# Performance work log

Hardware: AMD Instinct MI355X
Metric: run time of the kernel (lower is better)

Reference implementation:

```python
import jax, jax.numpy as jnp
import numpy as np

NUM_HEADS = 12


def _rel_lookup(rel_pos, size):
    # q_size == k_size == size, table length == 2*size-1: pure gather, no interp
    idx = jnp.arange(size)[:, None] - jnp.arange(size)[None, :] + (size - 1)
    return rel_pos[idx]  # (size, size, head_dim)


def setup_inputs() -> dict:
    key = jax.random.key(0)
    ks = jax.random.split(key, 7)
    B, H, W, C = 8, 32, 32, 768
    return {
        "x": jax.random.normal(ks[0], (B, H, W, C), dtype=jnp.float32),
        "w_qkv": jax.random.normal(ks[1], (C, 3 * C), dtype=jnp.float32) * 0.02,
        "b_qkv": jax.random.normal(ks[2], (3 * C,), dtype=jnp.float32) * 0.02,
        "w_proj": jax.random.normal(ks[3], (C, C), dtype=jnp.float32) * 0.02,
        "b_proj": jax.random.normal(ks[4], (C,), dtype=jnp.float32) * 0.02,
        "rel_pos_h": jax.random.normal(ks[5], (2 * H - 1, C // NUM_HEADS), dtype=jnp.float32) * 0.02,
        "rel_pos_w": jax.random.normal(ks[6], (2 * W - 1, C // NUM_HEADS), dtype=jnp.float32) * 0.02,
    }


def reference(x, w_qkv, b_qkv, w_proj, b_proj, rel_pos_h, rel_pos_w):
    B, H, W, C = x.shape
    nh = NUM_HEADS
    hd = C // nh
    scale = hd ** -0.5

    qkv = x @ w_qkv + b_qkv  # (B,H,W,3C)
    qkv = qkv.reshape(B, H * W, 3, nh, hd).transpose(2, 0, 3, 1, 4)
    qkv = qkv.reshape(3, B * nh, H * W, hd)
    q, k, v = qkv[0], qkv[1], qkv[2]  # each (B*nh, HW, hd)

    attn = jnp.einsum('bqd,bkd->bqk', q * scale, k)  # (B*nh, HW, HW)

    Rh = _rel_lookup(rel_pos_h, H)  # (H,H,hd)
    Rw = _rel_lookup(rel_pos_w, W)  # (W,W,hd)
    r_q = q.reshape(B * nh, H, W, hd)
    rel_h = jnp.einsum('bhwc,hkc->bhwk', r_q, Rh)  # (B*nh,H,W,H)
    rel_w = jnp.einsum('bhwc,wkc->bhwk', r_q, Rw)  # (B*nh,H,W,W)
    attn = (attn.reshape(B * nh, H, W, H, W)
            + rel_h[:, :, :, :, None]
            + rel_w[:, :, :, None, :]).reshape(B * nh, H * W, H * W)

    attn = jax.nn.softmax(attn, axis=-1)
    out = jnp.einsum('bqk,bkd->bqd', attn, v)  # (B*nh, HW, hd)
    out = out.reshape(B, nh, H, W, hd).transpose(0, 2, 3, 1, 4).reshape(B, H, W, C)
    return out @ w_proj + b_proj
```

## Files before the change

kernel.cpp:

```cpp
#include <hip/hip_runtime.h>

typedef unsigned short u16;
typedef unsigned int u32;
typedef __attribute__((ext_vector_type(8))) short short8;
typedef __attribute__((ext_vector_type(4))) float f32x4;
typedef __attribute__((ext_vector_type(4))) u32 u32x4;

__device__ __forceinline__ u16 f2bf(float f) {
  u32 u = __float_as_uint(f);
  return (u16)((u + 0x7FFFu + ((u >> 16) & 1u)) >> 16);
}
__device__ __forceinline__ float bf2f(u16 u) { return __uint_as_float(((u32)u) << 16); }
__device__ __forceinline__ f32x4 zero4() { f32x4 z = {0.f, 0.f, 0.f, 0.f}; return z; }

__device__ __forceinline__ u32 cvt_pk_bf16(float lo, float hi) {
  u32 r;
  asm("v_cvt_pk_bf16_f32 %0, %1, %2" : "=v"(r) : "v"(lo), "v"(hi));
  return r;
}

__device__ __forceinline__ void g2lds16(const void* g, void* l) {
  __builtin_amdgcn_global_load_lds((const __attribute__((address_space(1))) void*)g,
                                   (__attribute__((address_space(3))) void*)l, 16, 0, 0);
}

#define LOG2E 1.44269504088896340736f

__global__ __launch_bounds__(256) void cvt_x_kernel(const float* __restrict__ in,
                                                    u16* __restrict__ out, int n4) {
  int i = blockIdx.x * 256 + threadIdx.x;
  if (i >= n4) return;
  float4 v = ((const float4*)in)[i];
  ushort4 o;
  o.x = f2bf(v.x); o.y = f2bf(v.y); o.z = f2bf(v.z); o.w = f2bf(v.w);
  ((ushort4*)out)[i] = o;
}

__global__ __launch_bounds__(256) void transp_cvt_kernel(const float* __restrict__ in,
                                                         u16* __restrict__ out, int K, int N) {
  __shared__ float t[32][33];
  int n0 = blockIdx.x * 32, k0 = blockIdx.y * 32;
  int tx = threadIdx.x & 31, ty = threadIdx.x >> 5;
#pragma unroll
  for (int r = 0; r < 4; ++r)
    t[ty + r * 8][tx] = in[(size_t)(k0 + ty + r * 8) * N + n0 + tx];
  __syncthreads();
#pragma unroll
  for (int r = 0; r < 4; ++r)
    out[(size_t)(n0 + ty + r * 8) * K + k0 + tx] = f2bf(t[tx][ty + r * 8]);
}

template <int EPI>
__global__ __launch_bounds__(256, 3) void gemm_bt_kernel(
    const u16* __restrict__ A, const u16* __restrict__ Bt, const float* __restrict__ bias,
    int M, int N, int K,
    u16* __restrict__ q_out, u16* __restrict__ k_out, u16* __restrict__ vT_out,
    float* __restrict__ f_out) {
  __shared__ __align__(16) u16 As[2 * 128 * 32];
  __shared__ __align__(16) u16 Bs[2 * 128 * 32];
  const int tid = threadIdx.x;
  const int w = tid >> 6, lane = tid & 63;

  const int nwg = gridDim.x * gridDim.y;
  const int flat = blockIdx.y * gridDim.x + blockIdx.x;
  const int wg = (flat & 7) * (nwg >> 3) + (flat >> 3);
  const int bx = wg % gridDim.x, by = wg / gridDim.x;
  const int m0 = by * 128, n0 = bx * 128;
  const int wm0 = (w >> 1) * 64, wn0 = (w & 1) * 64;

  f32x4 acc[4][4];
#pragma unroll
  for (int i = 0; i < 4; ++i)
#pragma unroll
    for (int j = 0; j < 4; ++j) acc[i][j] = zero4();

  const int sRow = lane >> 2;
  const int sChunk = ((lane & 3) ^ ((lane >> 3) & 3)) * 8;
  const int cw = ((lane >> 4) << 4) ^ (((lane >> 1) & 3) << 4);
  const int g = lane >> 4, lc = lane & 15;
  const int lr = g << 2;

#define GSTAGE(buf, ktS)                                                                   \
  do {                                                                                     \
    _Pragma("unroll") for (int jj = 0; jj < 4; ++jj) {                                     \
      int i = w + jj * 4;                                                                  \
      if (i < 8)                                                                           \
        g2lds16(A + (size_t)(m0 + i * 16 + sRow) * K + (ktS) + sChunk,                     \
                (char*)As + (buf) * 8192 + i * 1024);                                      \
      else                                                                                 \
        g2lds16(Bt + (size_t)(n0 + (i - 8) * 16 + sRow) * K + (ktS) + sChunk,              \
                (char*)Bs + (buf) * 8192 + (i - 8) * 1024);                                \
    }                                                                                      \
  } while (0)

  const int nk = K >> 5;
  GSTAGE(0, 0);
  GSTAGE(1, 32);
  asm volatile("s_waitcnt vmcnt(4)" ::: "memory");
  __builtin_amdgcn_sched_barrier(0);
  __builtin_amdgcn_s_barrier();

  for (int kti = 0; kti < nk; ++kti) {
    const int cur = kti & 1;
    short8 af[4], bfr[4];
#pragma unroll
    for (int r = 0; r < 4; ++r) {
      af[r] = *(const short8*)((const char*)As + cur * 8192 + (wm0 + r * 16 + lc) * 64 + cw);
      bfr[r] = *(const short8*)((const char*)Bs + cur * 8192 + (wn0 + r * 16 + lc) * 64 + cw);
    }
    __builtin_amdgcn_s_setprio(1);
#pragma unroll
    for (int i = 0; i < 4; ++i)
#pragma unroll
      for (int j = 0; j < 4; ++j)
        acc[i][j] = __builtin_amdgcn_mfma_f32_16x16x32_bf16(af[i], bfr[j], acc[i][j], 0, 0, 0);
    __builtin_amdgcn_s_setprio(0);

    asm volatile("s_waitcnt lgkmcnt(0)" ::: "memory");
    __builtin_amdgcn_sched_barrier(0);
    __builtin_amdgcn_s_barrier();

    if (kti + 2 < nk) {
      GSTAGE(cur, (kti + 2) << 5);
      asm volatile("s_waitcnt vmcnt(4)" ::: "memory");
    } else {
      asm volatile("s_waitcnt vmcnt(0)" ::: "memory");
    }
    __builtin_amdgcn_sched_barrier(0);
    __builtin_amdgcn_s_barrier();
  }
#undef GSTAGE

#pragma unroll
  for (int j = 0; j < 4; ++j) {
    int n = n0 + wn0 + j * 16 + lc;
    float bv = bias[n];
    if (EPI == 0) {
      int three = n / 768;
      int rem = n - three * 768;
      int head = rem >> 6, d = rem & 63;
#pragma unroll
      for (int i = 0; i < 4; ++i) {
        if (three == 2) {
          int t0 = ((m0 + wm0 + i * 16 + lr) & 1023);
          int bb = (m0 + wm0 + i * 16 + lr) >> 10;
          size_t bh = (size_t)bb * 12 + head;
          ushort4 ov;
          ov.x = f2bf(acc[i][j][0] + bv);
          ov.y = f2bf(acc[i][j][1] + bv);
          ov.z = f2bf(acc[i][j][2] + bv);
          ov.w = f2bf(acc[i][j][3] + bv);
          *(ushort4*)(vT_out + (bh * 64 + d) * 1024 + t0) = ov;
        } else {
#pragma unroll
          for (int r = 0; r < 4; ++r) {
            int m = m0 + wm0 + i * 16 + lr + r;
            int bb = m >> 10, t = m & 1023;
            size_t bh = (size_t)bb * 12 + head;
            float val = acc[i][j][r] + bv;
            if (three == 0)
              q_out[(bh * 1024 + t) * 64 + d] = f2bf(val * (0.125f * LOG2E));
            else
              k_out[(bh * 1024 + t) * 64 + d] = f2bf(val);
          }
        }
      }
    } else {
#pragma unroll
      for (int i = 0; i < 4; ++i)
#pragma unroll
        for (int r = 0; r < 4; ++r) {
          int m = m0 + wm0 + i * 16 + lr + r;
          f_out[(size_t)m * N + n] = acc[i][j][r] + bv;
        }
    }
  }
}

__global__ __launch_bounds__(256) void rel_kernel(const u16* __restrict__ qs,
                                                  const float* __restrict__ rph,
                                                  const float* __restrict__ rpw,
                                                  float* __restrict__ relh,
                                                  float* __restrict__ relw) {
  __shared__ __align__(16) float Ts[63 * 68];
  __shared__ __align__(16) u16 Qs[32 * 72];
  const int tid = threadIdx.x;
  const int h = blockIdx.x, bh = blockIdx.y;
  const int mode = blockIdx.z;
  const float* table = mode ? rpw : rph;
  float* out = mode ? relw : relh;
  for (int i = tid; i < (63 * 64) / 4; i += 256) {
    float4 v = ((const float4*)table)[i];
    int row = i >> 4, col = (i & 15) * 4;
    *(float4*)(Ts + row * 68 + col) = v;
  }
  const u16* qrow = qs + ((size_t)bh * 1024 + h * 32) * 64;
  for (int i = tid; i < (32 * 64) / 8; i += 256) {
    uint4 v = ((const uint4*)qrow)[i];
    int row = i >> 3, col = (i & 7) * 8;
    *(uint4*)(Qs + row * 72 + col) = v;
  }
  __syncthreads();
  const int w = tid >> 3;
  const int kx = tid & 7;
  const int base = mode ? w : h;
  float acc0 = 0.f, acc1 = 0.f, acc2 = 0.f, acc3 = 0.f;
  const u16* qp = Qs + w * 72;
#pragma unroll
  for (int dc = 0; dc < 8; ++dc) {
    uint4 qv = *(const uint4*)(qp + dc * 8);
    float qf[8];
    qf[0] = bf2f((u16)(qv.x & 0xffff)); qf[1] = bf2f((u16)(qv.x >> 16));
    qf[2] = bf2f((u16)(qv.y & 0xffff)); qf[3] = bf2f((u16)(qv.y >> 16));
    qf[4] = bf2f((u16)(qv.z & 0xffff)); qf[5] = bf2f((u16)(qv.z >> 16));
    qf[6] = bf2f((u16)(qv.w & 0xffff)); qf[7] = bf2f((u16)(qv.w >> 16));
#pragma unroll
    for (int jj = 0; jj < 4; ++jj) {
      int row = base - (kx + 8 * jj) + 31;
      const float* tp = Ts + row * 68 + dc * 8;
      float4 p0 = ((const float4*)tp)[0];
      float4 p1 = ((const float4*)tp)[1];
      float s = qf[0] * p0.x + qf[1] * p0.y + qf[2] * p0.z + qf[3] * p0.w +
                qf[4] * p1.x + qf[5] * p1.y + qf[6] * p1.z + qf[7] * p1.w;
      if (jj == 0) acc0 += s;
      else if (jj == 1) acc1 += s;
      else if (jj == 2) acc2 += s;
      else acc3 += s;
    }
  }
  float* op = out + ((size_t)bh * 1024 + h * 32 + w) * 32 + kx;
  op[0] = acc0 * 8.f;
  op[8] = acc1 * 8.f;
  op[16] = acc2 * 8.f;
  op[24] = acc3 * 8.f;
}

__global__ __launch_bounds__(256) void flash_kernel(
    const u16* __restrict__ qs, const u16* __restrict__ kb, const u16* __restrict__ vT,
    const float* __restrict__ relh, const float* __restrict__ relw, u16* __restrict__ ao) {
  __shared__ __align__(16) u16 Ks[2 * 64 * 64];
  __shared__ __align__(16) u16 Vs[2 * 64 * 64];
  __shared__ __align__(16) float RhS[64 * 33];
  __shared__ __align__(16) u32 PpT[4][32 * 20];
  const int tid = threadIdx.x, wv = tid >> 6, lane = tid & 63;
  const int nwg = gridDim.x * gridDim.y;
  const int flat = blockIdx.y * gridDim.x + blockIdx.x;
  const int wg = (flat & 7) * (nwg >> 3) + (flat >> 3);
  const int qt = wg & 15, bh = wg >> 4;
  const int q0 = qt * 64;
  const int g = lane >> 4, lc = lane & 15;

  const float* rh_g = relh + ((size_t)bh * 1024 + q0) * 32;
  for (int i = tid; i < 64 * 32; i += 256) RhS[(i >> 5) * 33 + (i & 31)] = rh_g[i];

  const size_t qbase = ((size_t)bh * 1024 + q0 + wv * 16 + lc) * 64;
  short8 aq0 = *(const short8*)(qs + qbase + g * 8);
  short8 aq1 = *(const short8*)(qs + qbase + 32 + g * 8);

  const float* rwp = relw + ((size_t)bh * 1024 + q0 + wv * 16 + lc) * 32 + 4 * g;
  float4 rw0 = *(const float4*)(rwp);
  float4 rw1 = *(const float4*)(rwp + 16);
  float rwr[8] = {rw0.x, rw0.y, rw0.z, rw0.w, rw1.x, rw1.y, rw1.z, rw1.w};

  f32x4 o[4];
#pragma unroll
  for (int ct = 0; ct < 4; ++ct) o[ct] = zero4();
  float lsum = 0.f;
  const int rhbase = (wv * 16 + lc) * 33;

  const int stgRow = lane >> 3;
  const int stgChunk = ((lane & 7) ^ (lane >> 3)) * 8;
  u32* pt = &PpT[wv][0];

#define STAGE(buf, ktS)                                                                   \
  do {                                                                                    \
    const int k0s = (ktS) * 64;                                                           \
    _Pragma("unroll") for (int jj = 0; jj < 4; ++jj) {                                    \
      int i = wv + jj * 4;                                                                \
      if (i < 8)                                                                          \
        g2lds16(kb + ((size_t)bh * 1024 + k0s + i * 8 + stgRow) * 64 + stgChunk,          \
                (char*)Ks + (buf) * 8192 + i * 1024);                                     \
      else                                                                                \
        g2lds16(vT + ((size_t)bh * 64 + (i - 8) * 8 + stgRow) * 1024 + k0s + stgChunk,    \
                (char*)Vs + (buf) * 8192 + (i - 8) * 1024);                               \
    }                                                                                     \
  } while (0)

  STAGE(0, 0);
  __syncthreads();

  for (int kt = 0; kt < 16; ++kt) {
    const int cur = kt & 1;
    if (kt < 15) STAGE(cur ^ 1, kt + 1);

    f32x4 s[4];
    __builtin_amdgcn_s_setprio(1);
#pragma unroll
    for (int ct = 0; ct < 4; ++ct) {
      int key = ct * 16 + lc;
      int sw = (key & 7) << 4;
      const char* kp = (const char*)Ks + cur * 8192 + key * 128;
      short8 kf0 = *(const short8*)(kp + ((g * 16) ^ sw));
      short8 kf1 = *(const short8*)(kp + ((64 + g * 16) ^ sw));
      f32x4 z = zero4();
      z = __builtin_amdgcn_mfma_f32_16x16x32_bf16(kf0, aq0, z, 0, 0, 0);
      z = __builtin_amdgcn_mfma_f32_16x16x32_bf16(kf1, aq1, z, 0, 0, 0);
      s[ct] = z;
    }
    __builtin_amdgcn_s_setprio(0);

    float rh0 = RhS[rhbase + kt * 2 + 0];
    float rh1 = RhS[rhbase + kt * 2 + 1];
    float pr[4][4];
#pragma unroll
    for (int ct = 0; ct < 4; ++ct)
#pragma unroll
      for (int r = 0; r < 4; ++r)
        pr[ct][r] = __builtin_amdgcn_exp2f(s[ct][r] + (ct < 2 ? rh0 : rh1) +
                                           rwr[(ct & 1) * 4 + r]);

    lsum += ((pr[0][0] + pr[0][1]) + (pr[0][2] + pr[0][3])) +
            ((pr[1][0] + pr[1][1]) + (pr[1][2] + pr[1][3])) +
            ((pr[2][0] + pr[2][1]) + (pr[2][2] + pr[2][3])) +
            ((pr[3][0] + pr[3][1]) + (pr[3][2] + pr[3][3]));

#pragma unroll
    for (int ct = 0; ct < 4; ++ct) {
      u32 w0 = cvt_pk_bf16(pr[ct][0], pr[ct][1]);
      u32 w1 = cvt_pk_bf16(pr[ct][2], pr[ct][3]);
      pt[(8 * ct + 2 * g + 0) * 20 + lc] = w0;
      pt[(8 * ct + 2 * g + 1) * 20 + lc] = w1;
    }

    union { u32x4 u; short8 s; } pb0, pb1;
#pragma unroll
    for (int p = 0; p < 4; ++p) {
      pb0.u[p] = pt[(4 * g + p) * 20 + lc];
      pb1.u[p] = pt[(16 + 4 * g + p) * 20 + lc];
    }

    __builtin_amdgcn_s_setprio(1);
#pragma unroll
    for (int ct = 0; ct < 4; ++ct) {
      int d = ct * 16 + lc;
      int sw = (d & 7) << 4;
      const char* vp = (const char*)Vs + cur * 8192 + d * 128;
      short8 vf0 = *(const short8*)(vp + ((g * 16) ^ sw));
      short8 vf1 = *(const short8*)(vp + ((64 + g * 16) ^ sw));
      o[ct] = __builtin_amdgcn_mfma_f32_16x16x32_bf16(vf0, pb0.s, o[ct], 0, 0, 0);
      o[ct] = __builtin_amdgcn_mfma_f32_16x16x32_bf16(vf1, pb1.s, o[ct], 0, 0, 0);
    }
    __builtin_amdgcn_s_setprio(0);

    __syncthreads();
  }

  lsum += __shfl_xor(lsum, 16);
  lsum += __shfl_xor(lsum, 32);
  float inv = 1.0f / lsum;

  const int b_ = bh / 12, head = bh - b_ * 12;
  u16* op = ao + ((size_t)b_ * 1024 + q0 + wv * 16 + lc) * 768 + head * 64 + 4 * g;
#pragma unroll
  for (int ct = 0; ct < 4; ++ct) {
    ushort4 ov;
    ov.x = f2bf(o[ct][0] * inv);
    ov.y = f2bf(o[ct][1] * inv);
    ov.z = f2bf(o[ct][2] * inv);
    ov.w = f2bf(o[ct][3] * inv);
    *(ushort4*)(op + ct * 16) = ov;
  }
#undef STAGE
}

extern "C" void kernel_launch(void* const* d_in, const int* in_sizes, int n_in,
                              void* d_out, int out_size, void* d_ws, size_t ws_size,
                              hipStream_t stream) {
  const float* x = (const float*)d_in[0];
  const float* w_qkv = (const float*)d_in[1];
  const float* b_qkv = (const float*)d_in[2];
  const float* w_proj = (const float*)d_in[3];
  const float* b_proj = (const float*)d_in[4];
  const float* rph = (const float*)d_in[5];
  const float* rpw = (const float*)d_in[6];
  (void)in_sizes; (void)n_in; (void)out_size; (void)ws_size;

  char* ws = (char*)d_ws;
  size_t off = 0;
  auto alloc = [&](size_t bytes) {
    void* p = ws + off;
    off += (bytes + 255) & ~(size_t)255;
    return p;
  };
  u16* xb = (u16*)alloc((size_t)8192 * 768 * 2);
  float* relh = (float*)xb;
  u16* wqkvT = (u16*)alloc((size_t)2304 * 768 * 2);
  u16* wprojT = (u16*)alloc((size_t)768 * 768 * 2);
  u16* qsb = (u16*)alloc((size_t)96 * 1024 * 64 * 2);
  u16* kbb = (u16*)alloc((size_t)96 * 1024 * 64 * 2);
  u16* vTb = (u16*)alloc((size_t)96 * 64 * 1024 * 2);
  float* relw = (float*)alloc((size_t)96 * 1024 * 32 * 4);
  u16* ao = (u16*)alloc((size_t)8192 * 768 * 2);

  cvt_x_kernel<<<dim3(8192 * 768 / 4 / 256), 256, 0, stream>>>(x, xb, 8192 * 768 / 4);
  transp_cvt_kernel<<<dim3(2304 / 32, 768 / 32), 256, 0, stream>>>(w_qkv, wqkvT, 768, 2304);
  transp_cvt_kernel<<<dim3(768 / 32, 768 / 32), 256, 0, stream>>>(w_proj, wprojT, 768, 768);
  gemm_bt_kernel<0><<<dim3(2304 / 128, 8192 / 128), 256, 0, stream>>>(
      xb, wqkvT, b_qkv, 8192, 2304, 768, qsb, kbb, vTb, nullptr);
  rel_kernel<<<dim3(32, 96, 2), 256, 0, stream>>>(qsb, rph, rpw, relh, relw);
  flash_kernel<<<dim3(16, 96), 256, 0, stream>>>(qsb, kbb, vTb, relh, relw, ao);
  gemm_bt_kernel<1><<<dim3(768 / 128, 8192 / 128), 256, 0, stream>>>(
      ao, wprojT, b_proj, 8192, 768, 768, nullptr, nullptr, nullptr, (float*)d_out);
}
```

Baseline: 157.6 us.

## Use 256x256-tile, 512-thread GEMM with 64-wide K steps for QKV projection

Replaces the 128x128 templated GEMM for the QKV projection with a dedicated kernel that uses 256x256 output tiles, 8 waves, a 64-element K step, XOR-swizzled LDS and four MFMA phases per K step with setprio. The aim is more operand reuse per global load and fewer loop iterations on the largest GEMM. The projection GEMM keeps the old 128x128 kernel, specialized to the plain fp32 output epilogue. The cost is a grid of only 9x32=288 workgroups, which may leave compute units partly idle, plus higher register pressure from the 8x4 accumulator array.

```diff
diff --git a/kernel.cpp b/kernel.cpp
--- a/kernel.cpp
+++ b/kernel.cpp
@@ -50,12 +50,156 @@
     out[(size_t)(n0 + ty + r * 8) * K + k0 + tx] = f2bf(t[tx][ty + r * 8]);
 }
 
-template <int EPI>
-__global__ __launch_bounds__(256, 3) void gemm_bt_kernel(
+__global__ __launch_bounds__(512, 2) void gemm256_kernel(
     const u16* __restrict__ A, const u16* __restrict__ Bt, const float* __restrict__ bias,
     int M, int N, int K,
-    u16* __restrict__ q_out, u16* __restrict__ k_out, u16* __restrict__ vT_out,
-    float* __restrict__ f_out) {
+    u16* __restrict__ q_out, u16* __restrict__ k_out, u16* __restrict__ vT_out) {
+  __shared__ __align__(16) u16 As[2 * 256 * 64];
+  __shared__ __align__(16) u16 Bs[2 * 256 * 64];
+  const int tid = threadIdx.x;
+  const int wid = tid >> 6, lane = tid & 63;
+  const int wm = wid >> 2, wn = wid & 3;
+
+  const int nwg = gridDim.x * gridDim.y;
+  const int flat = blockIdx.y * gridDim.x + blockIdx.x;
+  const int wg = (flat & 7) * (nwg >> 3) + (flat >> 3);
+  const int bx = wg % gridDim.x, by = wg / gridDim.x;
+  const int m0 = by * 256, n0 = bx * 256;
+
+  const int g = lane >> 4, lc = lane & 15;
+  const int lr = g << 2;
+  const int sChunk = ((tid & 7) ^ ((tid >> 3) & 7)) * 8;
+
+  f32x4 acc[8][4];
+#pragma unroll
+  for (int i = 0; i < 8; ++i)
+#pragma unroll
+    for (int j = 0; j < 4; ++j) acc[i][j] = zero4();
+
+#define STAGE_A(buf, half, ktS)                                                          \
+  do {                                                                                   \
+    _Pragma("unroll") for (int l = 0; l < 2; ++l)                                        \
+        g2lds16(A + (size_t)(m0 + (half) * 128 + l * 64 + (tid >> 3)) * K + (ktS) +      \
+                    sChunk,                                                              \
+                (char*)As + (buf) * 32768 + (half) * 16384 + l * 8192 + tid * 16);       \
+  } while (0)
+#define STAGE_B(buf, half, ktS)                                                          \
+  do {                                                                                   \
+    _Pragma("unroll") for (int l = 0; l < 2; ++l)                                        \
+        g2lds16(Bt + (size_t)(n0 + (half) * 128 + l * 64 + (tid >> 3)) * K + (ktS) +     \
+                    sChunk,                                                              \
+                (char*)Bs + (buf) * 32768 + (half) * 16384 + l * 8192 + tid * 16);       \
+  } while (0)
+
+#define PHASE(B_, MQ, NQ)                                                                \
+  do {                                                                                   \
+    short8 af[4][2], bfr[2][2];                                                          \
+    _Pragma("unroll") for (int rr = 0; rr < 4; ++rr) {                                   \
+      int row = wm * 128 + (MQ) * 64 + rr * 16 + lc;                                     \
+      const char* base = (const char*)As + (B_) * 32768 + row * 128;                     \
+      af[rr][0] = *(const short8*)(base + (((0 + g) ^ (lc & 7)) << 4));                  \
+      af[rr][1] = *(const short8*)(base + (((4 + g) ^ (lc & 7)) << 4));                  \
+    }                                                                                    \
+    _Pragma("unroll") for (int jj = 0; jj < 2; ++jj) {                                   \
+      int row = wn * 64 + (NQ) * 32 + jj * 16 + lc;                                      \
+      const char* base = (const char*)Bs + (B_) * 32768 + row * 128;                     \
+      bfr[jj][0] = *(const short8*)(base + (((0 + g) ^ (lc & 7)) << 4));                 \
+      bfr[jj][1] = *(const short8*)(base + (((4 + g) ^ (lc & 7)) << 4));                 \
+    }                                                                                    \
+    __builtin_amdgcn_sched_barrier(0);                                                   \
+    __builtin_amdgcn_s_barrier();                                                        \
+    asm volatile("s_waitcnt lgkmcnt(0)" ::: "memory");                                   \
+    __builtin_amdgcn_sched_barrier(0);                                                   \
+    __builtin_amdgcn_s_setprio(1);                                                       \
+    _Pragma("unroll") for (int ks = 0; ks < 2; ++ks)                                     \
+        _Pragma("unroll") for (int rr = 0; rr < 4; ++rr)                                 \
+            _Pragma("unroll") for (int jj = 0; jj < 2; ++jj) acc[(MQ)*4 + rr][(NQ)*2 +   \
+                                                                jj] =                    \
+                __builtin_amdgcn_mfma_f32_16x16x32_bf16(af[rr][ks], bfr[jj][ks],         \
+                                                        acc[(MQ)*4 + rr][(NQ)*2 + jj],  \
+                                                        0, 0, 0);                        \
+    __builtin_amdgcn_s_setprio(0);                                                       \
+    __builtin_amdgcn_sched_barrier(0);                                                   \
+    __builtin_amdgcn_s_barrier();                                                        \
+    __builtin_amdgcn_sched_barrier(0);                                                   \
+  } while (0)
+
+  const int nk = K >> 6;
+  STAGE_A(0, 0, 0);
+  STAGE_A(0, 1, 0);
+  STAGE_B(0, 0, 0);
+  STAGE_B(0, 1, 0);
+  STAGE_A(1, 0, 64);
+  STAGE_A(1, 1, 64);
+  STAGE_B(1, 0, 64);
+  STAGE_B(1, 1, 64);
+  asm volatile("s_waitcnt vmcnt(8)" ::: "memory");
+  __builtin_amdgcn_sched_barrier(0);
+  __builtin_amdgcn_s_barrier();
+
+  for (int it = 0; it < nk; ++it) {
+    const int b = it & 1;
+    PHASE(b, 0, 0);
+    PHASE(b, 0, 1);
+    PHASE(b, 1, 0);
+    PHASE(b, 1, 1);
+    if (it + 2 < nk) {
+      const int kt2 = (it + 2) << 6;
+      STAGE_A(b, 0, kt2);
+      STAGE_A(b, 1, kt2);
+      STAGE_B(b, 0, kt2);
+      STAGE_B(b, 1, kt2);
+      asm volatile("s_waitcnt vmcnt(8)" ::: "memory");
+    } else if (it + 1 < nk) {
+      asm volatile("s_waitcnt vmcnt(0)" ::: "memory");
+    }
+    __builtin_amdgcn_sched_barrier(0);
+    __builtin_amdgcn_s_barrier();
+  }
+#undef PHASE
+#undef STAGE_A
+#undef STAGE_B
+
+#pragma unroll
+  for (int j = 0; j < 4; ++j) {
+    int n = n0 + wn * 64 + j * 16 + lc;
+    float bv = bias[n];
+    int three = n / 768;
+    int rem = n - three * 768;
+    int head = rem >> 6, d = rem & 63;
+#pragma unroll
+    for (int i = 0; i < 8; ++i) {
+      int mbase = m0 + wm * 128 + i * 16 + lr;
+      if (three == 2) {
+        int t0 = mbase & 1023;
+        int bb = mbase >> 10;
+        size_t bh = (size_t)bb * 12 + head;
+        ushort4 ov;
+        ov.x = f2bf(acc[i][j][0] + bv);
+        ov.y = f2bf(acc[i][j][1] + bv);
+        ov.z = f2bf(acc[i][j][2] + bv);
+        ov.w = f2bf(acc[i][j][3] + bv);
+        *(ushort4*)(vT_out + (bh * 64 + d) * 1024 + t0) = ov;
+      } else {
+#pragma unroll
+        for (int r = 0; r < 4; ++r) {
+          int m = mbase + r;
+          int bb = m >> 10, t = m & 1023;
+          size_t bh = (size_t)bb * 12 + head;
+          float val = acc[i][j][r] + bv;
+          if (three == 0)
+            q_out[(bh * 1024 + t) * 64 + d] = f2bf(val * (0.125f * LOG2E));
+          else
+            k_out[(bh * 1024 + t) * 64 + d] = f2bf(val);
+        }
+      }
+    }
+  }
+}
+
+__global__ __launch_bounds__(256, 3) void gemm_proj_kernel(
+    const u16* __restrict__ A, const u16* __restrict__ Bt, const float* __restrict__ bias,
+    int M, int N, int K, float* __restrict__ f_out) {
   __shared__ __align__(16) u16 As[2 * 128 * 32];
   __shared__ __align__(16) u16 Bs[2 * 128 * 32];
   const int tid = threadIdx.x;
@@ -135,45 +279,13 @@
   for (int j = 0; j < 4; ++j) {
     int n = n0 + wn0 + j * 16 + lc;
     float bv = bias[n];
-    if (EPI == 0) {
-      int three = n / 768;
-      int rem = n - three * 768;
-      int head = rem >> 6, d = rem & 63;
-#pragma unroll
-      for (int i = 0; i < 4; ++i) {
-        if (three == 2) {
-          int t0 = ((m0 + wm0 + i * 16 + lr) & 1023);
-          int bb = (m0 + wm0 + i * 16 + lr) >> 10;
-          size_t bh = (size_t)bb * 12 + head;
-          ushort4 ov;
-          ov.x = f2bf(acc[i][j][0] + bv);
-          ov.y = f2bf(acc[i][j][1] + bv);
-          ov.z = f2bf(acc[i][j][2] + bv);
-          ov.w = f2bf(acc[i][j][3] + bv);
-          *(ushort4*)(vT_out + (bh * 64 + d) * 1024 + t0) = ov;
-        } else {
-#pragma unroll
-          for (int r = 0; r < 4; ++r) {
-            int m = m0 + wm0 + i * 16 + lr + r;
-            int bb = m >> 10, t = m & 1023;
-            size_t bh = (size_t)bb * 12 + head;
-            float val = acc[i][j][r] + bv;
-            if (three == 0)
-              q_out[(bh * 1024 + t) * 64 + d] = f2bf(val * (0.125f * LOG2E));
-            else
-              k_out[(bh * 1024 + t) * 64 + d] = f2bf(val);
-          }
-        }
+#pragma unroll
+    for (int i = 0; i < 4; ++i)
+#pragma unroll
+      for (int r = 0; r < 4; ++r) {
+        int m = m0 + wm0 + i * 16 + lr + r;
+        f_out[(size_t)m * N + n] = acc[i][j][r] + bv;
       }
-    } else {
-#pragma unroll
-      for (int i = 0; i < 4; ++i)
-#pragma unroll
-        for (int r = 0; r < 4; ++r) {
-          int m = m0 + wm0 + i * 16 + lr + r;
-          f_out[(size_t)m * N + n] = acc[i][j][r] + bv;
-        }
-    }
   }
 }
 
@@ -405,10 +517,10 @@
   cvt_x_kernel<<<dim3(8192 * 768 / 4 / 256), 256, 0, stream>>>(x, xb, 8192 * 768 / 4);
   transp_cvt_kernel<<<dim3(2304 / 32, 768 / 32), 256, 0, stream>>>(w_qkv, wqkvT, 768, 2304);
   transp_cvt_kernel<<<dim3(768 / 32, 768 / 32), 256, 0, stream>>>(w_proj, wprojT, 768, 768);
-  gemm_bt_kernel<0><<<dim3(2304 / 128, 8192 / 128), 256, 0, stream>>>(
-      xb, wqkvT, b_qkv, 8192, 2304, 768, qsb, kbb, vTb, nullptr);
+  gemm256_kernel<<<dim3(2304 / 256, 8192 / 256), 512, 0, stream>>>(
+      xb, wqkvT, b_qkv, 8192, 2304, 768, qsb, kbb, vTb);
   rel_kernel<<<dim3(32, 96, 2), 256, 0, stream>>>(qsb, rph, rpw, relh, relw);
   flash_kernel<<<dim3(16, 96), 256, 0, stream>>>(qsb, kbb, vTb, relh, relw, ao);
-  gemm_bt_kernel<1><<<dim3(768 / 128, 8192 / 128), 256, 0, stream>>>(
-      ao, wprojT, b_proj, 8192, 768, 768, nullptr, nullptr, nullptr, (float*)d_out);
-}
+  gemm_proj_kernel<<<dim3(768 / 128, 8192 / 128), 256, 0, stream>>>(
+      ao, wprojT, b_proj, 8192, 768, 768, (float*)d_out);
+}
```

New measurement: 183.1 us. +16.2%, slower.
